# Kernel tuning notes

Measured on AMD Instinct MI355X. Metric: run time of the kernel, lower is better.

Reference implementation:

```python
import jax, jax.numpy as jnp
import numpy as np

B, T, N_EMBED = 16, 4096, 48
HEAD_SIZE, DIM = 8, 64  # dim = 2**n_wires, n_wires = 6


def setup_inputs() -> dict:
    key = jax.random.key(0)
    k1, k2, k3 = jax.random.split(key, 3)
    x = jax.random.normal(k1, (B, T, N_EMBED), dtype=jnp.float32)
    obs_re = jax.random.normal(k2, (HEAD_SIZE, DIM, DIM), dtype=jnp.float32)
    obs_im = jax.random.normal(k3, (HEAD_SIZE, DIM, DIM), dtype=jnp.float32)
    return {"x": x, "obs_re": obs_re, "obs_im": obs_im}


def reference(x, obs_re, obs_im):
    # x: (B, T, C) real; obs: (H, dim, dim) complex observables O'.
    b, t, c = x.shape
    h, dim, _ = obs_re.shape
    O = (obs_re + 1j * obs_im).astype(jnp.complex64)  # (h, dim, dim)
    # psi: zero-padded complex state, x loaded into first n_embed amplitudes
    psi = jnp.zeros((b * t, dim), dtype=jnp.complex64)
    psi = psi.at[:, :c].set(x.reshape(b * t, c).astype(jnp.complex64))
    # O_psi[h, n, i] = sum_j O[h, i, j] * psi[n, j]  (all heads in one batched GEMM)
    O_psi = jnp.einsum('hij,nj->hni', O, psi)
    # exp[n, h] = Re( psi^H O' psi )
    exp = jnp.einsum('ni,hni->nh', jnp.conj(psi), O_psi).real
    return exp.reshape(b, t, h).astype(jnp.float32)
```

## Files before the change

kernel.cpp:

```cpp
#include <hip/hip_runtime.h>


#define NTOK 65536
#define NHEAD 8
#define XSTRIDE 56
#define TPB 128

typedef __attribute__((ext_vector_type(8))) short short8;
typedef __attribute__((ext_vector_type(4))) short short4v;
typedef __attribute__((ext_vector_type(4))) float float4v;

static __device__ __forceinline__ short f2bf(float f) {
    unsigned int u = __builtin_bit_cast(unsigned int, f);
    u += 0x7FFFu + ((u >> 16) & 1u);
    return (short)(u >> 16);
}
static __device__ __forceinline__ float bf2f(short s) {
    return __builtin_bit_cast(float, ((unsigned int)(unsigned short)s) << 16);
}

__global__ void prep_frags(const float* __restrict__ obs, short* __restrict__ frags) {
    const int tid  = threadIdx.x;
    const int w    = tid >> 6, lane = tid & 63;
    const int q    = lane >> 4, c = lane & 15;
    const int h    = blockIdx.x * 4 + w;
    #pragma unroll
    for (int u = 0; u < 6; ++u) {
        const int kt = u / 3, it = u % 3;
        const int f  = h * 6 + u;
        const float4* src = (const float4*)(obs +
            ((size_t)(h * 64 + 16 * it + c) * 64 + 32 * kt + 8 * q));
        float4 v0 = src[0], v1 = src[1];
        short8 a;
        a[0] = f2bf(v0.x); a[1] = f2bf(v0.y); a[2] = f2bf(v0.z); a[3] = f2bf(v0.w);
        a[4] = f2bf(v1.x); a[5] = f2bf(v1.y); a[6] = f2bf(v1.z); a[7] = f2bf(v1.w);
        *(short8*)(frags + ((size_t)f * 64 + lane) * 8) = a;
    }
}

__global__ __launch_bounds__(256, 2) void qform_main(
    const short* __restrict__ frags,
    const float* __restrict__ x,
    float* __restrict__ out)
{
    __shared__ short a_lds[48 * 64 * 8];
    __shared__ short xl[TPB * XSTRIDE];

    const int tid  = threadIdx.x;
    const int w    = tid >> 6, lane = tid & 63;
    const int q    = lane >> 4, c = lane & 15;
    const int tb   = blockIdx.x * TPB;

    #pragma unroll
    for (int u = 0; u < 12; ++u) {
        const int f = u * 4 + w;
        short8 a = *(const short8*)(frags + ((size_t)f * 64 + lane) * 8);
        *(short8*)(a_lds + ((size_t)f * 64 + lane) * 8) = a;
    }

    #pragma unroll
    for (int s = 0; s < 6; ++s) {
        int idx = s * 256 + tid;
        int t = idx / 12, ch = idx % 12;
        float4 v = ((const float4*)x)[(size_t)tb * 12 + idx];
        short4v b;
        b.x = f2bf(v.x); b.y = f2bf(v.y); b.z = f2bf(v.z); b.w = f2bf(v.w);
        *(short4v*)(xl + t * XSTRIDE + ch * 4) = b;
    }
    __syncthreads();

    const int hbase = (w >> 1) * 4;
    const int gbase = (w & 1) * 4;

    short8 bfr[4][2];
    float  xe[4][3][4];
    #pragma unroll
    for (int g = 0; g < 4; ++g) {
        const int row = (gbase + g) * 16 + c;
        bfr[g][0] = *(const short8*)(xl + row * XSTRIDE + q * 8);
        if (q < 2)
            bfr[g][1] = *(const short8*)(xl + row * XSTRIDE + 32 + q * 8);
        else
            bfr[g][1] = (short8)0;
        #pragma unroll
        for (int it = 0; it < 3; ++it)
            #pragma unroll
            for (int r = 0; r < 4; ++r)
                xe[g][it][r] = bf2f(xl[row * XSTRIDE + 16 * it + 4 * q + r]);
    }

    float ph[4][4];
    #pragma unroll
    for (int hh = 0; hh < 4; ++hh) {
        const int h = hbase + hh;
        short8 A[6];
        #pragma unroll
        for (int u = 0; u < 6; ++u)
            A[u] = *(const short8*)(a_lds + ((size_t)(h * 6 + u) * 64 + lane) * 8);
        #pragma unroll
        for (int g = 0; g < 4; ++g) {
            float4v acc[3];
            #pragma unroll
            for (int it = 0; it < 3; ++it) {
                float4v z = {0.f, 0.f, 0.f, 0.f};
                acc[it] = __builtin_amdgcn_mfma_f32_16x16x32_bf16(A[it],     bfr[g][0], z,       0, 0, 0);
                acc[it] = __builtin_amdgcn_mfma_f32_16x16x32_bf16(A[3 + it], bfr[g][1], acc[it], 0, 0, 0);
            }
            float p = 0.f;
            #pragma unroll
            for (int it = 0; it < 3; ++it)
                #pragma unroll
                for (int r = 0; r < 4; ++r)
                    p += acc[it][r] * xe[g][it][r];
            p += __shfl_xor(p, 16, 64);
            p += __shfl_xor(p, 32, 64);
            ph[g][hh] = p;
        }
    }

    if (lane < 16) {
        #pragma unroll
        for (int g = 0; g < 4; ++g) {
            float4* o4 = (float4*)(out +
                (size_t)(tb + (gbase + g) * 16 + c) * NHEAD + hbase);
            o4[0] = make_float4(ph[g][0], ph[g][1], ph[g][2], ph[g][3]);
        }
    }
}

extern "C" void kernel_launch(void* const* d_in, const int* in_sizes, int n_in,
                              void* d_out, int out_size, void* d_ws, size_t ws_size,
                              hipStream_t stream) {
    const float* x      = (const float*)d_in[0];
    const float* obs_re = (const float*)d_in[1];
    float* out   = (float*)d_out;
    short* frags = (short*)d_ws;

    prep_frags<<<2, 256, 0, stream>>>(obs_re, frags);
    qform_main<<<NTOK / TPB, 256, 0, stream>>>(frags, x, out);
}
```

Before: 69.34 us.

## Fuse observable fragment prep into main kernel and double block size

Drops the separate prep kernel. Each of the 8 waves in a 512-thread block now converts one head's observable straight from global fp32 to bf16 MFMA fragments in LDS. Tokens per block double to 256, the x loads are issued before the observable conversion so their latency overlaps it, and the xe reads from LDS are vectorised. This removes a kernel launch and the workspace round trip, at the cost of every block redoing the obs conversion and of larger blocks lowering occupancy granularity.

```diff
diff --git a/kernel.cpp b/kernel.cpp
--- a/kernel.cpp
+++ b/kernel.cpp
@@ -4,7 +4,8 @@
 #define NTOK 65536
 #define NHEAD 8
 #define XSTRIDE 56
-#define TPB 128
+#define TPB 256
+#define NTHREADS 512
 
 typedef __attribute__((ext_vector_type(8))) short short8;
 typedef __attribute__((ext_vector_type(4))) short short4v;
@@ -19,28 +20,9 @@
     return __builtin_bit_cast(float, ((unsigned int)(unsigned short)s) << 16);
 }
 
-__global__ void prep_frags(const float* __restrict__ obs, short* __restrict__ frags) {
-    const int tid  = threadIdx.x;
-    const int w    = tid >> 6, lane = tid & 63;
-    const int q    = lane >> 4, c = lane & 15;
-    const int h    = blockIdx.x * 4 + w;
-    #pragma unroll
-    for (int u = 0; u < 6; ++u) {
-        const int kt = u / 3, it = u % 3;
-        const int f  = h * 6 + u;
-        const float4* src = (const float4*)(obs +
-            ((size_t)(h * 64 + 16 * it + c) * 64 + 32 * kt + 8 * q));
-        float4 v0 = src[0], v1 = src[1];
-        short8 a;
-        a[0] = f2bf(v0.x); a[1] = f2bf(v0.y); a[2] = f2bf(v0.z); a[3] = f2bf(v0.w);
-        a[4] = f2bf(v1.x); a[5] = f2bf(v1.y); a[6] = f2bf(v1.z); a[7] = f2bf(v1.w);
-        *(short8*)(frags + ((size_t)f * 64 + lane) * 8) = a;
-    }
-}
-
-__global__ __launch_bounds__(256, 2) void qform_main(
-    const short* __restrict__ frags,
+__global__ __launch_bounds__(NTHREADS, 2) void qform_fused(
     const float* __restrict__ x,
+    const float* __restrict__ obs,
     float* __restrict__ out)
 {
     __shared__ short a_lds[48 * 64 * 8];
@@ -51,26 +33,39 @@
     const int q    = lane >> 4, c = lane & 15;
     const int tb   = blockIdx.x * TPB;
 
+    float4 xv[6];
+    int    xt[6], xch[6];
     #pragma unroll
-    for (int u = 0; u < 12; ++u) {
-        const int f = u * 4 + w;
-        short8 a = *(const short8*)(frags + ((size_t)f * 64 + lane) * 8);
-        *(short8*)(a_lds + ((size_t)f * 64 + lane) * 8) = a;
+    for (int s = 0; s < 6; ++s) {
+        int idx = s * NTHREADS + tid;
+        xv[s]  = ((const float4*)x)[(size_t)tb * 12 + idx];
+        xt[s]  = idx / 12;
+        xch[s] = idx % 12;
+    }
+
+    #pragma unroll
+    for (int u = 0; u < 6; ++u) {
+        const int kt = u / 3, it = u % 3;
+        const float4* src = (const float4*)(obs +
+            ((size_t)(w * 64 + 16 * it + c) * 64 + 32 * kt + 8 * q));
+        float4 v0 = src[0], v1 = src[1];
+        short8 a;
+        a[0] = f2bf(v0.x); a[1] = f2bf(v0.y); a[2] = f2bf(v0.z); a[3] = f2bf(v0.w);
+        a[4] = f2bf(v1.x); a[5] = f2bf(v1.y); a[6] = f2bf(v1.z); a[7] = f2bf(v1.w);
+        *(short8*)(a_lds + ((size_t)(w * 6 + u) * 64 + lane) * 8) = a;
     }
 
     #pragma unroll
     for (int s = 0; s < 6; ++s) {
-        int idx = s * 256 + tid;
-        int t = idx / 12, ch = idx % 12;
-        float4 v = ((const float4*)x)[(size_t)tb * 12 + idx];
         short4v b;
-        b.x = f2bf(v.x); b.y = f2bf(v.y); b.z = f2bf(v.z); b.w = f2bf(v.w);
-        *(short4v*)(xl + t * XSTRIDE + ch * 4) = b;
+        b.x = f2bf(xv[s].x); b.y = f2bf(xv[s].y);
+        b.z = f2bf(xv[s].z); b.w = f2bf(xv[s].w);
+        *(short4v*)(xl + xt[s] * XSTRIDE + xch[s] * 4) = b;
     }
     __syncthreads();
 
-    const int hbase = (w >> 1) * 4;
-    const int gbase = (w & 1) * 4;
+    const int hbase = (w >> 2) * 4;
+    const int gbase = (w & 3) * 4;
 
     short8 bfr[4][2];
     float  xe[4][3][4];
@@ -83,10 +78,11 @@
         else
             bfr[g][1] = (short8)0;
         #pragma unroll
-        for (int it = 0; it < 3; ++it)
-            #pragma unroll
-            for (int r = 0; r < 4; ++r)
-                xe[g][it][r] = bf2f(xl[row * XSTRIDE + 16 * it + 4 * q + r]);
+        for (int it = 0; it < 3; ++it) {
+            short4v xs = *(const short4v*)(xl + row * XSTRIDE + 16 * it + 4 * q);
+            xe[g][it][0] = bf2f(xs.x); xe[g][it][1] = bf2f(xs.y);
+            xe[g][it][2] = bf2f(xs.z); xe[g][it][3] = bf2f(xs.w);
+        }
     }
 
     float ph[4][4];
@@ -133,9 +129,7 @@
                               hipStream_t stream) {
     const float* x      = (const float*)d_in[0];
     const float* obs_re = (const float*)d_in[1];
-    float* out   = (float*)d_out;
-    short* frags = (short*)d_ws;
+    float* out = (float*)d_out;
 
-    prep_frags<<<2, 256, 0, stream>>>(obs_re, frags);
-    qform_main<<<NTOK / TPB, 256, 0, stream>>>(frags, x, out);
+    qform_fused<<<NTOK / TPB, NTHREADS, 0, stream>>>(x, obs_re, out);
 }
```

Measured after the change: 68.66 us. About the same (-1.0%).
